# Performance work log

Hardware: AMD Instinct MI355X
Metric: run time of the kernel (lower is better)

Reference implementation:

```python
import jax, jax.numpy as jnp
import numpy as np

K = 3  # local attention window (kernel_size)


def setup_inputs() -> dict:
    key = jax.random.key(0)
    ks = jax.random.split(key, 10)
    B, C, S = 1, 128, 24
    scale = 1.0 / np.sqrt(C).astype(np.float32)
    x = jax.random.normal(ks[0], (B, C, S, S, S), dtype=jnp.float32)
    wq = jax.random.normal(ks[1], (C, C), dtype=jnp.float32) * scale
    bq = jax.random.normal(ks[2], (C,), dtype=jnp.float32) * 0.01
    wk = jax.random.normal(ks[3], (C, C), dtype=jnp.float32) * scale
    bk = jax.random.normal(ks[4], (C,), dtype=jnp.float32) * 0.01
    wv = jax.random.normal(ks[5], (C, C), dtype=jnp.float32) * scale
    bv = jax.random.normal(ks[6], (C,), dtype=jnp.float32) * 0.01
    rel_h = jax.random.normal(ks[7], (C // 2, K, 1, 1), dtype=jnp.float32)
    rel_w = jax.random.normal(ks[8], (C // 2, 1, K, 1), dtype=jnp.float32)
    rel_d = jax.random.normal(ks[9], (C // 2, 1, 1, K), dtype=jnp.float32)
    return {"x": x, "wq": wq, "bq": bq, "wk": wk, "bk": bk,
            "wv": wv, "bv": bv, "rel_h": rel_h, "rel_w": rel_w, "rel_d": rel_d}


def reference(x, wq, bq, wk, bk, wv, bv, rel_h, rel_w, rel_d):
    B, C, H, W, D = x.shape
    p = (K - 1) // 2
    pad = ((0, 0), (0, 0), (p, K - 1 - p), (p, K - 1 - p), (p, K - 1 - p))
    xp = jnp.pad(x, pad)

    # 1x1x1 Conv3d == per-voxel linear map
    conv1 = lambda y, w, b: jnp.einsum('bchwd,oc->bohwd', y, w) + b[None, :, None, None, None]
    q = conv1(x, wq, bq)          # [B,C,H,W,D]
    kf = conv1(xp, wk, bk)        # padded
    vf = conv1(xp, wv, bv)

    def unfold(y):
        # torch unfold(2,K,1).unfold(3,K,1).unfold(4,K,1) flattened row-major (i,j,l)
        pats = [y[:, :, i:i + H, j:j + W, l:l + D]
                for i in range(K) for j in range(K) for l in range(K)]
        return jnp.stack(pats, axis=-1)  # [B,C,H,W,D,K^3]

    kw = unfold(kf)
    vw = unfold(vf)

    # q^T k per voxel over the K^3 window (num_heads=1 so head split is identity)
    qk = jnp.einsum('bchwd,bchwds->bhwds', q, kw)  # [B,H,W,D,27]

    # Faithful to einsum('bhxytdz,cijk->bhxytijk'): d,z,c are all summed
    # independently -> (sum_d q) * (sum_c rel) broadcast over the window.
    qsum = jnp.sum(q, axis=1)                         # [B,H,W,D]
    bias = rel_h.sum(0) + rel_w.sum(0) + rel_d.sum(0)  # [K,K,K] via broadcast
    qk = qk.reshape(B, H, W, D, K, K, K) + qsum[..., None, None, None] * bias

    attn = jax.nn.softmax(qk.reshape(B, H, W, D, K ** 3), axis=-1)
    out = jnp.einsum('bhwds,bchwds->bhwdc', attn, vw)  # [B,H,W,D,C]
    # torch: [B,1,H,W,D,1,C].reshape(B,-1,H,W,D) -- same row-major flatten here
    return out.reshape(B, -1, H, W, D)
```

## Files before the change

### kernel.cpp

```cpp
#include <hip/hip_runtime.h>

#define CCH 128
#define SV 24
#define NVOX 13824

typedef unsigned short u16;
typedef unsigned int   u32;

__device__ __forceinline__ u16 f2bf(float f) {
    u32 x = __float_as_uint(f);
    u32 r = x + 0x7fffu + ((x >> 16) & 1u);
    return (u16)(r >> 16);
}
__device__ __forceinline__ void cvt4b(uint2 r, float* f) {
    f[0] = __uint_as_float(r.x << 16); f[1] = __uint_as_float(r.x & 0xffff0000u);
    f[2] = __uint_as_float(r.y << 16); f[3] = __uint_as_float(r.y & 0xffff0000u);
}

__global__ __launch_bounds__(256) void proj_kernel(
    const float* __restrict__ x,
    const float* __restrict__ wq, const float* __restrict__ bq,
    const float* __restrict__ wk, const float* __restrict__ bk,
    const float* __restrict__ wv, const float* __restrict__ bv,
    const float* __restrict__ relh, const float* __restrict__ relw,
    const float* __restrict__ reld,
    float* __restrict__ qout, float* __restrict__ kws, u16* __restrict__ vws,
    float* __restrict__ biasW)
{
    const int m = blockIdx.y;
    const float* __restrict__ w = (m == 0) ? wq : (m == 1) ? wk : wv;
    const float* __restrict__ b = (m == 0) ? bq : (m == 1) ? bk : bv;

    __shared__ float Xs[32][64];
    __shared__ float Ws[32][64];

    const int tid  = threadIdx.x;
    const int vox0 = blockIdx.x * 64;
    const int oblk = blockIdx.z * 64;
    const int v0   = (tid & 15) * 4;
    const int o0   = (tid >> 4) * 4;

    const int xc  = tid >> 3;
    const int xv  = (tid & 7) * 4;
    const int wo  = tid & 63;
    const int wkh = (tid >> 6) * 8;

    float acc[4][4] = {{0.f}};

    for (int k0 = 0; k0 < CCH; k0 += 32) {
        {
            const float* src = x + (size_t)(k0 + xc) * NVOX + vox0 + xv;
            const float4 a0 = *(const float4*)src;
            const float4 a1 = *(const float4*)(src + 32);
            *(float4*)&Xs[xc][xv]      = a0;
            *(float4*)&Xs[xc][xv + 32] = a1;
        }
        {
            const float* src = w + (size_t)(oblk + wo) * CCH + k0 + wkh;
            const float4 b0 = *(const float4*)src;
            const float4 b1 = *(const float4*)(src + 4);
            Ws[wkh + 0][wo] = b0.x; Ws[wkh + 1][wo] = b0.y;
            Ws[wkh + 2][wo] = b0.z; Ws[wkh + 3][wo] = b0.w;
            Ws[wkh + 4][wo] = b1.x; Ws[wkh + 5][wo] = b1.y;
            Ws[wkh + 6][wo] = b1.z; Ws[wkh + 7][wo] = b1.w;
        }
        __syncthreads();

#pragma unroll
        for (int k = 0; k < 32; ++k) {
            const float4 xf = *(const float4*)&Xs[k][v0];
            const float4 wf = *(const float4*)&Ws[k][o0];
            const float xr[4] = {xf.x, xf.y, xf.z, xf.w};
            const float wr[4] = {wf.x, wf.y, wf.z, wf.w};
#pragma unroll
            for (int vv = 0; vv < 4; ++vv)
#pragma unroll
                for (int oo = 0; oo < 4; ++oo)
                    acc[vv][oo] = fmaf(xr[vv], wr[oo], acc[vv][oo]);
        }
        __syncthreads();
    }

    const float4 bf = *(const float4*)(b + oblk + o0);
    const float br[4] = {bf.x, bf.y, bf.z, bf.w};

#pragma unroll
    for (int vv = 0; vv < 4; ++vv) {
        float r[4];
#pragma unroll
        for (int oo = 0; oo < 4; ++oo) r[oo] = acc[vv][oo] + br[oo];
        const size_t row = (size_t)(vox0 + v0 + vv) * CCH + oblk + o0;
        if (m == 0) {
            float4 st = {r[0], r[1], r[2], r[3]};
            *(float4*)(qout + row) = st;
        } else if (m == 1) {
            float4 st = {r[0], r[1], r[2], r[3]};
            *(float4*)(kws + row) = st;
        } else {
            uint2 st;
            st.x = (u32)f2bf(r[0]) | ((u32)f2bf(r[1]) << 16);
            st.y = (u32)f2bf(r[2]) | ((u32)f2bf(r[3]) << 16);
            *(uint2*)(vws + row) = st;
        }
    }

    if (blockIdx.x == 0 && blockIdx.z == 0) {
        if (m == 1 && tid < CCH) kws[(size_t)NVOX * CCH + tid] = bk[tid];
        if (m == 2 && tid < CCH) vws[(size_t)NVOX * CCH + tid] = f2bf(bv[tid]);
        if (m == 1 && tid < 27) {
            const int i = tid / 9, j = (tid / 3) % 3, l = tid % 3;
            float s = 0.f;
            for (int c = 0; c < 64; ++c)
                s += relh[c * 3 + i] + relw[c * 3 + j] + reld[c * 3 + l];
            biasW[tid] = s;
        }
    }
}

__device__ __forceinline__ int nbr_off(int h, int w, int d, int s, int ch) {
    const int nh = h + s / 9 - 1;
    const int nw = w + (s / 3) % 3 - 1;
    const int nd = d + s % 3 - 1;
    const bool ok = ((unsigned)nh < (unsigned)SV) &&
                    ((unsigned)nw < (unsigned)SV) &&
                    ((unsigned)nd < (unsigned)SV);
    const int idx = ok ? ((nh * SV + nw) * SV + nd) : NVOX;
    return idx * CCH + ch;
}

__global__ __launch_bounds__(256) void attn_kernel(
    float* __restrict__ qo, const float* __restrict__ kws,
    const u16* __restrict__ vws, const float* __restrict__ biasW)
{
    const int tid  = threadIdx.x;
    const int lane = tid & 31;
    const int vox  = blockIdx.x * 8 + (tid >> 5);
    const int h    = vox / 576;
    const int rem  = vox - h * 576;
    const int w    = rem / 24;
    const int d    = rem - w * 24;
    const int ch   = lane * 4;

    const float4 q4 = *(const float4*)(qo + (size_t)vox * CCH + ch);
    const float qr[4] = {q4.x, q4.y, q4.z, q4.w};

    float qs = qr[0] + qr[1] + qr[2] + qr[3];
#pragma unroll
    for (int mm = 1; mm < 32; mm <<= 1) qs += __shfl_xor(qs, mm, 64);

    float ps[27];
#pragma unroll
    for (int sb = 0; sb < 27; sb += 9) {
        float4 kf[9];
#pragma unroll
        for (int j = 0; j < 9; ++j)
            kf[j] = *(const float4*)(kws + nbr_off(h, w, d, sb + j, ch));
#pragma unroll
        for (int j = 0; j < 9; ++j) {
            float p = qr[0] * kf[j].x;
            p = fmaf(qr[1], kf[j].y, p);
            p = fmaf(qr[2], kf[j].z, p);
            p = fmaf(qr[3], kf[j].w, p);
            ps[sb + j] = p;
        }
    }

#pragma unroll
    for (int mm = 1; mm < 32; mm <<= 1) {
#pragma unroll
        for (int s = 0; s < 27; ++s) ps[s] += __shfl_xor(ps[s], mm, 64);
    }

#pragma unroll
    for (int s = 0; s < 27; ++s) ps[s] = fmaf(qs, biasW[s], ps[s]);

    float mx = ps[0];
#pragma unroll
    for (int s = 1; s < 27; ++s) mx = fmaxf(mx, ps[s]);
    float sum = 0.f;
#pragma unroll
    for (int s = 0; s < 27; ++s) { ps[s] = __expf(ps[s] - mx); sum += ps[s]; }
    const float inv = 1.f / sum;
#pragma unroll
    for (int s = 0; s < 27; ++s) ps[s] *= inv;

    float o[4] = {0.f, 0.f, 0.f, 0.f};
#pragma unroll
    for (int sb = 0; sb < 27; sb += 9) {
        uint2 vf[9];
#pragma unroll
        for (int j = 0; j < 9; ++j)
            vf[j] = *(const uint2*)(vws + nbr_off(h, w, d, sb + j, ch));
#pragma unroll
        for (int j = 0; j < 9; ++j) {
            float f[4];
            cvt4b(vf[j], f);
            const float a = ps[sb + j];
            o[0] = fmaf(a, f[0], o[0]); o[1] = fmaf(a, f[1], o[1]);
            o[2] = fmaf(a, f[2], o[2]); o[3] = fmaf(a, f[3], o[3]);
        }
    }

    float4 st = {o[0], o[1], o[2], o[3]};
    *(float4*)(qo + (size_t)vox * CCH + ch) = st;
}

extern "C" void kernel_launch(void* const* d_in, const int* in_sizes, int n_in,
                              void* d_out, int out_size, void* d_ws,
                              size_t ws_size, hipStream_t stream)
{
    const float* x    = (const float*)d_in[0];
    const float* wq   = (const float*)d_in[1];
    const float* bq   = (const float*)d_in[2];
    const float* wk   = (const float*)d_in[3];
    const float* bk   = (const float*)d_in[4];
    const float* wv   = (const float*)d_in[5];
    const float* bv   = (const float*)d_in[6];
    const float* relh = (const float*)d_in[7];
    const float* relw = (const float*)d_in[8];
    const float* reld = (const float*)d_in[9];

    float* kws   = (float*)d_ws;
    u16*   vws   = (u16*)(kws + (size_t)(NVOX + 1) * CCH);
    float* biasW = (float*)(vws + (size_t)(NVOX + 1) * CCH);

    dim3 pgrid(NVOX / 64, 3, 2);
    proj_kernel<<<pgrid, 256, 0, stream>>>(x, wq, bq, wk, bk, wv, bv,
                                           relh, relw, reld,
                                           (float*)d_out, kws, vws, biasW);
    attn_kernel<<<NVOX / 8, 256, 0, stream>>>((float*)d_out, kws, vws, biasW);
}
```

Measured before the change: 115.1 us.

## Restructure attention into padded channel-pair layout with separate QK and PV kernels

Projections now write Q, K and V in a channel-pair-major interleaved layout. K and V go into a spatially padded volume whose halo holds the bias values, so neighbor lookups need no bounds checks. The single attention kernel is split into a QK/softmax kernel, which writes attention weights to a workspace, and a PV kernel. Each thread now handles one voxel and loops over channels instead of reducing across lanes with shuffles. The projection tile grows to 128 outputs per block with padded shared memory, and V goes back to fp32 from bf16. The extra kernel launch and the attention-weight round trip add memory traffic and fixed cost.

```diff
diff --git a/kernel.cpp b/kernel.cpp
--- a/kernel.cpp
+++ b/kernel.cpp
@@ -1,20 +1,22 @@
 #include <hip/hip_runtime.h>
 
-#define CCH 128
-#define SV 24
-#define NVOX 13824
-
-typedef unsigned short u16;
-typedef unsigned int   u32;
-
-__device__ __forceinline__ u16 f2bf(float f) {
-    u32 x = __float_as_uint(f);
-    u32 r = x + 0x7fffu + ((x >> 16) & 1u);
-    return (u16)(r >> 16);
-}
-__device__ __forceinline__ void cvt4b(uint2 r, float* f) {
-    f[0] = __uint_as_float(r.x << 16); f[1] = __uint_as_float(r.x & 0xffff0000u);
-    f[2] = __uint_as_float(r.y << 16); f[3] = __uint_as_float(r.y & 0xffff0000u);
+#define CCH   128
+#define NC2   64
+#define SV    24
+#define NVOX  13824
+#define SH    728
+#define SW    28
+#define PVOL  18928
+
+__device__ __forceinline__ int pad_base(int lin) {
+    const int h = lin / 576;
+    const int r = lin - h * 576;
+    const int w = r / 24;
+    const int d = r - w * 24;
+    return (h + 1) * SH + (w + 1) * SW + d + 2;
+}
+__device__ __forceinline__ int slot_off(int s) {
+    return (s / 9 - 1) * SH + ((s / 3) % 3 - 1) * SW + (s % 3 - 1);
 }
 
 __global__ __launch_bounds__(256) void proj_kernel(
@@ -24,185 +26,229 @@
     const float* __restrict__ wv, const float* __restrict__ bv,
     const float* __restrict__ relh, const float* __restrict__ relw,
     const float* __restrict__ reld,
-    float* __restrict__ qout, float* __restrict__ kws, u16* __restrict__ vws,
+    float* __restrict__ qI, float* __restrict__ kI, float* __restrict__ vI,
     float* __restrict__ biasW)
 {
-    const int m = blockIdx.y;
-    const float* __restrict__ w = (m == 0) ? wq : (m == 1) ? wk : wv;
-    const float* __restrict__ b = (m == 0) ? bq : (m == 1) ? bk : bv;
-
-    __shared__ float Xs[32][64];
-    __shared__ float Ws[32][64];
-
-    const int tid  = threadIdx.x;
-    const int vox0 = blockIdx.x * 64;
-    const int oblk = blockIdx.z * 64;
-    const int v0   = (tid & 15) * 4;
-    const int o0   = (tid >> 4) * 4;
-
-    const int xc  = tid >> 3;
-    const int xv  = (tid & 7) * 4;
-    const int wo  = tid & 63;
-    const int wkh = (tid >> 6) * 8;
-
-    float acc[4][4] = {{0.f}};
-
-    for (int k0 = 0; k0 < CCH; k0 += 32) {
-        {
-            const float* src = x + (size_t)(k0 + xc) * NVOX + vox0 + xv;
-            const float4 a0 = *(const float4*)src;
-            const float4 a1 = *(const float4*)(src + 32);
-            *(float4*)&Xs[xc][xv]      = a0;
-            *(float4*)&Xs[xc][xv + 32] = a1;
-        }
-        {
-            const float* src = w + (size_t)(oblk + wo) * CCH + k0 + wkh;
-            const float4 b0 = *(const float4*)src;
-            const float4 b1 = *(const float4*)(src + 4);
-            Ws[wkh + 0][wo] = b0.x; Ws[wkh + 1][wo] = b0.y;
-            Ws[wkh + 2][wo] = b0.z; Ws[wkh + 3][wo] = b0.w;
-            Ws[wkh + 4][wo] = b1.x; Ws[wkh + 5][wo] = b1.y;
-            Ws[wkh + 6][wo] = b1.z; Ws[wkh + 7][wo] = b1.w;
-        }
-        __syncthreads();
-
-#pragma unroll
-        for (int k = 0; k < 32; ++k) {
-            const float4 xf = *(const float4*)&Xs[k][v0];
-            const float4 wf = *(const float4*)&Ws[k][o0];
-            const float xr[4] = {xf.x, xf.y, xf.z, xf.w};
-            const float wr[4] = {wf.x, wf.y, wf.z, wf.w};
-#pragma unroll
-            for (int vv = 0; vv < 4; ++vv)
-#pragma unroll
-                for (int oo = 0; oo < 4; ++oo)
-                    acc[vv][oo] = fmaf(xr[vv], wr[oo], acc[vv][oo]);
-        }
-        __syncthreads();
-    }
-
-    const float4 bf = *(const float4*)(b + oblk + o0);
-    const float br[4] = {bf.x, bf.y, bf.z, bf.w};
-
-#pragma unroll
-    for (int vv = 0; vv < 4; ++vv) {
-        float r[4];
-#pragma unroll
-        for (int oo = 0; oo < 4; ++oo) r[oo] = acc[vv][oo] + br[oo];
-        const size_t row = (size_t)(vox0 + v0 + vv) * CCH + oblk + o0;
-        if (m == 0) {
-            float4 st = {r[0], r[1], r[2], r[3]};
-            *(float4*)(qout + row) = st;
-        } else if (m == 1) {
-            float4 st = {r[0], r[1], r[2], r[3]};
-            *(float4*)(kws + row) = st;
-        } else {
-            uint2 st;
-            st.x = (u32)f2bf(r[0]) | ((u32)f2bf(r[1]) << 16);
-            st.y = (u32)f2bf(r[2]) | ((u32)f2bf(r[3]) << 16);
-            *(uint2*)(vws + row) = st;
-        }
-    }
-
-    if (blockIdx.x == 0 && blockIdx.z == 0) {
-        if (m == 1 && tid < CCH) kws[(size_t)NVOX * CCH + tid] = bk[tid];
-        if (m == 2 && tid < CCH) vws[(size_t)NVOX * CCH + tid] = f2bf(bv[tid]);
-        if (m == 1 && tid < 27) {
+    const int m   = blockIdx.y;
+    const int tid = threadIdx.x;
+
+    if (m == 3) {
+        if (blockIdx.x == 0 && tid < 27) {
             const int i = tid / 9, j = (tid / 3) % 3, l = tid % 3;
             float s = 0.f;
             for (int c = 0; c < 64; ++c)
                 s += relh[c * 3 + i] + relw[c * 3 + j] + reld[c * 3 + l];
             biasW[tid] = s;
         }
-    }
-}
-
-__device__ __forceinline__ int nbr_off(int h, int w, int d, int s, int ch) {
-    const int nh = h + s / 9 - 1;
-    const int nw = w + (s / 3) % 3 - 1;
-    const int nd = d + s % 3 - 1;
-    const bool ok = ((unsigned)nh < (unsigned)SV) &&
-                    ((unsigned)nw < (unsigned)SV) &&
-                    ((unsigned)nd < (unsigned)SV);
-    const int idx = ok ? ((nh * SV + nw) * SV + nd) : NVOX;
-    return idx * CCH + ch;
-}
-
-__global__ __launch_bounds__(256) void attn_kernel(
-    float* __restrict__ qo, const float* __restrict__ kws,
-    const u16* __restrict__ vws, const float* __restrict__ biasW)
-{
+        const int g = blockIdx.x * 256 + tid;
+        if (g < PVOL) {
+            const int ph = g / SH;
+            const int r  = g - ph * SH;
+            const int pw = r / SW;
+            const int pd = r - pw * SW;
+            const bool interior = ((unsigned)(ph - 1) < 24u) &&
+                                  ((unsigned)(pw - 1) < 24u) &&
+                                  ((unsigned)(pd - 2) < 24u);
+            if (!interior) {
+                float2* kp2 = (float2*)kI;
+                float2* vp2 = (float2*)vI;
+                for (int c2 = 0; c2 < NC2; ++c2) {
+                    float2 kv = {bk[2 * c2], bk[2 * c2 + 1]};
+                    float2 vv = {bv[2 * c2], bv[2 * c2 + 1]};
+                    kp2[(size_t)c2 * PVOL + g] = kv;
+                    vp2[(size_t)c2 * PVOL + g] = vv;
+                }
+            }
+        }
+        return;
+    }
+
+    const float* __restrict__ w = (m == 0) ? wq : (m == 1) ? wk : wv;
+    const float* __restrict__ b = (m == 0) ? bq : (m == 1) ? bk : bv;
+
+    __shared__ float Xs[32][68];
+    __shared__ float Ws[32][132];
+
+    const int vox0 = blockIdx.x * 64;
+    const int o0   = (tid >> 4) * 8;
+    const int v0   = (tid & 15) * 4;
+
+    const int xr    = tid >> 3;
+    const int xc4   = (tid & 7) * 8;
+    const int o_r   = tid >> 1;
+    const int c_off = (tid & 1) * 16;
+
+    float acc[8][4] = {{0.f}};
+
+    for (int k0 = 0; k0 < CCH; k0 += 32) {
+        const float* xs = x + (size_t)(k0 + xr) * NVOX + vox0 + xc4;
+        const float4 a0 = *(const float4*)xs;
+        const float4 a1 = *(const float4*)(xs + 4);
+        const float* wsrc = w + o_r * CCH + k0 + c_off;
+        const float4 b0 = *(const float4*)wsrc;
+        const float4 b1 = *(const float4*)(wsrc + 4);
+        const float4 b2 = *(const float4*)(wsrc + 8);
+        const float4 b3 = *(const float4*)(wsrc + 12);
+
+        __syncthreads();
+        *(float4*)&Xs[xr][xc4]     = a0;
+        *(float4*)&Xs[xr][xc4 + 4] = a1;
+        Ws[c_off +  0][o_r] = b0.x; Ws[c_off +  1][o_r] = b0.y;
+        Ws[c_off +  2][o_r] = b0.z; Ws[c_off +  3][o_r] = b0.w;
+        Ws[c_off +  4][o_r] = b1.x; Ws[c_off +  5][o_r] = b1.y;
+        Ws[c_off +  6][o_r] = b1.z; Ws[c_off +  7][o_r] = b1.w;
+        Ws[c_off +  8][o_r] = b2.x; Ws[c_off +  9][o_r] = b2.y;
+        Ws[c_off + 10][o_r] = b2.z; Ws[c_off + 11][o_r] = b2.w;
+        Ws[c_off + 12][o_r] = b3.x; Ws[c_off + 13][o_r] = b3.y;
+        Ws[c_off + 14][o_r] = b3.z; Ws[c_off + 15][o_r] = b3.w;
+        __syncthreads();
+
+#pragma unroll
+        for (int k = 0; k < 32; ++k) {
+            const float4 wA = *(const float4*)&Ws[k][o0];
+            const float4 wB = *(const float4*)&Ws[k][o0 + 4];
+            const float4 xv = *(const float4*)&Xs[k][v0];
+            const float wr[8] = {wA.x, wA.y, wA.z, wA.w,
+                                 wB.x, wB.y, wB.z, wB.w};
+            const float xr4[4] = {xv.x, xv.y, xv.z, xv.w};
+#pragma unroll
+            for (int i = 0; i < 8; ++i)
+#pragma unroll
+                for (int v = 0; v < 4; ++v)
+                    acc[i][v] = fmaf(wr[i], xr4[v], acc[i][v]);
+        }
+    }
+
+    float br[8];
+    *(float4*)br       = *(const float4*)(b + o0);
+    *(float4*)(br + 4) = *(const float4*)(b + o0 + 4);
+    float r[8][4];
+#pragma unroll
+    for (int i = 0; i < 8; ++i)
+#pragma unroll
+        for (int v = 0; v < 4; ++v) r[i][v] = acc[i][v] + br[i];
+
+    const int lin0 = vox0 + v0;
+    if (m == 0) {
+        float2* q2 = (float2*)qI;
+#pragma unroll
+        for (int t = 0; t < 4; ++t) {
+            const int c2 = (o0 >> 1) + t;
+#pragma unroll
+            for (int vp = 0; vp < 2; ++vp) {
+                const int v = vp * 2;
+                float4 st = {r[2 * t][v],     r[2 * t + 1][v],
+                             r[2 * t][v + 1], r[2 * t + 1][v + 1]};
+                *(float4*)&q2[(size_t)c2 * NVOX + lin0 + v] = st;
+            }
+        }
+    } else {
+        float2* p2 = (float2*)((m == 1) ? kI : vI);
+        const int pb = pad_base(lin0);
+#pragma unroll
+        for (int t = 0; t < 4; ++t) {
+            const int c2 = (o0 >> 1) + t;
+#pragma unroll
+            for (int vp = 0; vp < 2; ++vp) {
+                const int v = vp * 2;
+                float4 st = {r[2 * t][v],     r[2 * t + 1][v],
+                             r[2 * t][v + 1], r[2 * t + 1][v + 1]};
+                *(float4*)&p2[(size_t)c2 * PVOL + pb + v] = st;
+            }
+        }
+    }
+}
+
+__global__ __launch_bounds__(192) void qk_kernel(
+    const float* __restrict__ qI, const float* __restrict__ kI,
+    const float* __restrict__ biasW, float* __restrict__ aws)
+{
+    __shared__ float psh[27][64];
     const int tid  = threadIdx.x;
-    const int lane = tid & 31;
-    const int vox  = blockIdx.x * 8 + (tid >> 5);
-    const int h    = vox / 576;
-    const int rem  = vox - h * 576;
-    const int w    = rem / 24;
-    const int d    = rem - w * 24;
-    const int ch   = lane * 4;
-
-    const float4 q4 = *(const float4*)(qo + (size_t)vox * CCH + ch);
-    const float qr[4] = {q4.x, q4.y, q4.z, q4.w};
-
-    float qs = qr[0] + qr[1] + qr[2] + qr[3];
-#pragma unroll
-    for (int mm = 1; mm < 32; mm <<= 1) qs += __shfl_xor(qs, mm, 64);
-
-    float ps[27];
-#pragma unroll
-    for (int sb = 0; sb < 27; sb += 9) {
-        float4 kf[9];
-#pragma unroll
-        for (int j = 0; j < 9; ++j)
-            kf[j] = *(const float4*)(kws + nbr_off(h, w, d, sb + j, ch));
+    const int lane = tid & 63;
+    const int s0   = (tid >> 6) * 9;
+    const int vox  = blockIdx.x * 64 + lane;
+    const int pb   = pad_base(vox);
+
+    int koff[9];
+#pragma unroll
+    for (int j = 0; j < 9; ++j) koff[j] = pb + slot_off(s0 + j);
+
+    const float2* q2 = (const float2*)qI;
+    const float2* k2 = (const float2*)kI;
+
+    float ps[9] = {0.f, 0.f, 0.f, 0.f, 0.f, 0.f, 0.f, 0.f, 0.f};
+    float qs = 0.f;
+    for (int c2 = 0; c2 < NC2; ++c2) {
+        const float2 q = q2[(size_t)c2 * NVOX + vox];
+        qs += q.x + q.y;
+        const size_t base = (size_t)c2 * PVOL;
 #pragma unroll
         for (int j = 0; j < 9; ++j) {
-            float p = qr[0] * kf[j].x;
-            p = fmaf(qr[1], kf[j].y, p);
-            p = fmaf(qr[2], kf[j].z, p);
-            p = fmaf(qr[3], kf[j].w, p);
-            ps[sb + j] = p;
-        }
-    }
-
-#pragma unroll
-    for (int mm = 1; mm < 32; mm <<= 1) {
-#pragma unroll
-        for (int s = 0; s < 27; ++s) ps[s] += __shfl_xor(ps[s], mm, 64);
-    }
-
-#pragma unroll
-    for (int s = 0; s < 27; ++s) ps[s] = fmaf(qs, biasW[s], ps[s]);
-
-    float mx = ps[0];
-#pragma unroll
-    for (int s = 1; s < 27; ++s) mx = fmaxf(mx, ps[s]);
-    float sum = 0.f;
-#pragma unroll
-    for (int s = 0; s < 27; ++s) { ps[s] = __expf(ps[s] - mx); sum += ps[s]; }
-    const float inv = 1.f / sum;
-#pragma unroll
-    for (int s = 0; s < 27; ++s) ps[s] *= inv;
-
-    float o[4] = {0.f, 0.f, 0.f, 0.f};
-#pragma unroll
-    for (int sb = 0; sb < 27; sb += 9) {
-        uint2 vf[9];
-#pragma unroll
-        for (int j = 0; j < 9; ++j)
-            vf[j] = *(const uint2*)(vws + nbr_off(h, w, d, sb + j, ch));
-#pragma unroll
-        for (int j = 0; j < 9; ++j) {
-            float f[4];
-            cvt4b(vf[j], f);
-            const float a = ps[sb + j];
-            o[0] = fmaf(a, f[0], o[0]); o[1] = fmaf(a, f[1], o[1]);
-            o[2] = fmaf(a, f[2], o[2]); o[3] = fmaf(a, f[3], o[3]);
-        }
-    }
-
-    float4 st = {o[0], o[1], o[2], o[3]};
-    *(float4*)(qo + (size_t)vox * CCH + ch) = st;
+            const float2 k = k2[base + koff[j]];
+            ps[j] = fmaf(q.x, k.x, ps[j]);
+            ps[j] = fmaf(q.y, k.y, ps[j]);
+        }
+    }
+#pragma unroll
+    for (int j = 0; j < 9; ++j)
+        psh[s0 + j][lane] = fmaf(qs, biasW[s0 + j], ps[j]);
+    __syncthreads();
+
+    if (tid < 64) {
+        float v[27];
+        float mx = -1e30f;
+#pragma unroll
+        for (int s = 0; s < 27; ++s) { v[s] = psh[s][tid]; mx = fmaxf(mx, v[s]); }
+        float sum = 0.f;
+#pragma unroll
+        for (int s = 0; s < 27; ++s) { v[s] = __expf(v[s] - mx); sum += v[s]; }
+        const float inv = 1.f / sum;
+        const int gv = blockIdx.x * 64 + tid;
+#pragma unroll
+        for (int s = 0; s < 27; ++s) aws[s * NVOX + gv] = v[s] * inv;
+    }
+}
+
+__global__ __launch_bounds__(256) void pv_kernel(
+    const float* __restrict__ vI, const float* __restrict__ aws,
+    float* __restrict__ out)
+{
+    const int tid  = threadIdx.x;
+    const int lane = tid & 63;
+    const int wv   = tid >> 6;
+    const int vox  = blockIdx.x * 64 + lane;
+    const int pb   = pad_base(vox);
+
+    int voff[27];
+#pragma unroll
+    for (int s = 0; s < 27; ++s) voff[s] = pb + slot_off(s);
+
+    float a[27];
+#pragma unroll
+    for (int s = 0; s < 27; ++s) a[s] = aws[s * NVOX + vox];
+
+    const float2* v2 = (const float2*)vI;
+    float* orow = out + (size_t)vox * CCH;
+
+#pragma unroll
+    for (int i = 0; i < 16; i += 2) {
+        const int c2a = wv * 16 + i;
+        float2 acc0 = {0.f, 0.f}, acc1 = {0.f, 0.f};
+        const size_t ba = (size_t)c2a * PVOL;
+        const size_t bb = ba + PVOL;
+#pragma unroll
+        for (int s = 0; s < 27; ++s) {
+            const float2 va = v2[ba + voff[s]];
+            const float2 vb = v2[bb + voff[s]];
+            acc0.x = fmaf(a[s], va.x, acc0.x);
+            acc0.y = fmaf(a[s], va.y, acc0.y);
+            acc1.x = fmaf(a[s], vb.x, acc1.x);
+            acc1.y = fmaf(a[s], vb.y, acc1.y);
+        }
+        float4 st = {acc0.x, acc0.y, acc1.x, acc1.y};
+        *(float4*)(orow + c2a * 2) = st;
+    }
 }
 
 extern "C" void kernel_launch(void* const* d_in, const int* in_sizes, int n_in,
@@ -220,13 +266,16 @@
     const float* relw = (const float*)d_in[8];
     const float* reld = (const float*)d_in[9];
 
-    float* kws   = (float*)d_ws;
-    u16*   vws   = (u16*)(kws + (size_t)(NVOX + 1) * CCH);
-    float* biasW = (float*)(vws + (size_t)(NVOX + 1) * CCH);
-
-    dim3 pgrid(NVOX / 64, 3, 2);
+    float* qI    = (float*)d_ws;
+    float* kI    = qI + (size_t)CCH * NVOX;
+    float* vI    = kI + (size_t)CCH * PVOL;
+    float* aws   = vI + (size_t)CCH * PVOL;
+    float* biasW = aws + (size_t)27 * NVOX;
+
+    dim3 pgrid(NVOX / 64, 4);
     proj_kernel<<<pgrid, 256, 0, stream>>>(x, wq, bq, wk, bk, wv, bv,
                                            relh, relw, reld,
-                                           (float*)d_out, kws, vws, biasW);
-    attn_kernel<<<NVOX / 8, 256, 0, stream>>>((float*)d_out, kws, vws, biasW);
-}
+                                           qI, kI, vI, biasW);
+    qk_kernel<<<NVOX / 64, 192, 0, stream>>>(qI, kI, biasW, aws);
+    pv_kernel<<<NVOX / 64, 256, 0, stream>>>(vI, aws, (float*)d_out);
+}
```

New measurement: 161.0 us. 39.9% more time.
